# Kernel tuning notes

Measured on AMD Instinct MI355X. Metric: run time of the kernel, lower is better.

Reference implementation:

```python
import jax, jax.numpy as jnp
import numpy as np

N_NODES = 100000
N_EDGES = 3200000
D_IN = 512
D_OUT = 512


def setup_inputs() -> dict:
    key = jax.random.key(0)
    k1, k2, k3, k4, k5 = jax.random.split(key, 5)
    features = jax.random.normal(k1, (N_NODES, D_IN), dtype=jnp.float32)
    edge_src = jax.random.randint(k2, (N_EDGES,), 0, N_NODES, dtype=jnp.int32)
    edge_dst = jnp.sort(jax.random.randint(k3, (N_EDGES,), 0, N_NODES, dtype=jnp.int32))
    # normalized-adjacency-like positive edge weights
    edge_weight = jax.random.uniform(k4, (N_EDGES,), dtype=jnp.float32)
    # xavier_uniform_ for weight [D_IN, D_OUT]
    limit = float(np.sqrt(6.0 / (D_IN + D_OUT)))
    weight = jax.random.uniform(k5, (D_IN, D_OUT), dtype=jnp.float32,
                                minval=-limit, maxval=limit)
    return {
        "features": features,
        "weight": weight,
        "edge_src": edge_src,
        "edge_dst": edge_dst,
        "edge_weight": edge_weight,
        "times": 3,
    }


def reference(features, weight, edge_src, edge_dst, edge_weight, times):
    n_nodes = features.shape[0]
    # dense feature transform: support = features @ W
    support = features @ weight  # [N, D_OUT]

    def spmm(x):
        # out[dst] += w * x[src]  (one hop of sparse adjacency propagation)
        msgs = x[edge_src] * edge_weight[:, None]  # [E, D_OUT]
        return jax.ops.segment_sum(msgs, edge_dst, num_segments=n_nodes)

    output = spmm(support)
    for _ in range(times - 1):
        output = spmm(output)
    return output
```

## Files before the change

### kernel.cpp

```cpp
#include <hip/hip_runtime.h>

#define N_NODES_C 100000
#define N_EDGES_C 3200000
#define DDIM 512

typedef float v4f __attribute__((ext_vector_type(4)));
typedef unsigned int v4u __attribute__((ext_vector_type(4)));
typedef _Float16 v8hf __attribute__((ext_vector_type(8)));

__device__ inline unsigned short f2h(float f) {
    union { _Float16 h; unsigned short u; } v;
    v.h = (_Float16)f;
    return v.u;
}
__device__ inline float h2f(unsigned short s) {
    union { unsigned short u; _Float16 h; } v;
    v.u = s;
    return (float)v.h;
}

__device__ __forceinline__ void gload_lds16(const void* g, void* l) {
    __builtin_amdgcn_global_load_lds(
        (const __attribute__((address_space(1))) unsigned int*)(void*)(g),
        (__attribute__((address_space(3))) unsigned int*)(l),
        16, 0, 0);
}

__global__ __launch_bounds__(256) void build_rowptr(const int* __restrict__ dst,
                                                    int* __restrict__ rp) {
    int n = blockIdx.x * blockDim.x + threadIdx.x;
    if (n > N_NODES_C) return;
    int lo = 0, hi = N_EDGES_C;
    while (lo < hi) {
        int mid = (lo + hi) >> 1;
        if (dst[mid] < n) lo = mid + 1;
        else hi = mid;
    }
    rp[n] = lo;
}

__global__ __launch_bounds__(256) void convert_x(const v4f* __restrict__ X,
                                                 v4u* __restrict__ Xh) {
    const size_t i = (size_t)blockIdx.x * 256 + threadIdx.x;
    const v4f a = X[2 * i];
    const v4f b = X[2 * i + 1];
    v4u o;
    o.x = (unsigned)f2h(a.x) | ((unsigned)f2h(a.y) << 16);
    o.y = (unsigned)f2h(a.z) | ((unsigned)f2h(a.w) << 16);
    o.z = (unsigned)f2h(b.x) | ((unsigned)f2h(b.y) << 16);
    o.w = (unsigned)f2h(b.z) | ((unsigned)f2h(b.w) << 16);
    Xh[i] = o;
}

__global__ __launch_bounds__(256) void transpose_b(const float* __restrict__ B,
                                                   unsigned short* __restrict__ Bt) {
    __shared__ float t[32][33];
    const int bk = blockIdx.x * 32;
    const int bn = blockIdx.y * 32;
    const int x  = threadIdx.x & 31;
    const int y0 = threadIdx.x >> 5;
#pragma unroll
    for (int r = y0; r < 32; r += 8)
        t[r][x] = B[(size_t)(bk + r) * DDIM + bn + x];
    __syncthreads();
#pragma unroll
    for (int r = y0; r < 32; r += 8)
        Bt[(size_t)(bn + r) * DDIM + bk + x] = f2h(t[x][r]);
}

__global__ __launch_bounds__(256) void gemm3(const unsigned short* __restrict__ Ah,
                                             const unsigned short* __restrict__ Bt,
                                             unsigned short* __restrict__ C,
                                             int M) {
    __shared__ unsigned short sA[128 * 32];
    __shared__ unsigned short sB[128 * 32];

    const int tid  = threadIdx.x;
    const int lane = tid & 63;
    const int wave = tid >> 6;
    const int quad = lane >> 4;
    const int l16  = lane & 15;
    const int wr   = (wave >> 1) * 64;
    const int wc   = (wave & 1) * 64;
    const int m0   = blockIdx.x * 128;
    const int n0   = blockIdx.y * 128;

    int ar0 = m0 + (tid >> 2);
    int ar1 = ar0 + 64;
    if (ar0 >= M) ar0 = 0;
    if (ar1 >= M) ar1 = 0;
    const unsigned short* ga0 = Ah + (size_t)ar0 * DDIM + (tid & 3) * 8;
    const unsigned short* ga1 = Ah + (size_t)ar1 * DDIM + (tid & 3) * 8;
    const unsigned short* gb0 = Bt + (size_t)(n0 + (tid >> 2)) * DDIM + (tid & 3) * 8;
    const unsigned short* gb1 = gb0 + (size_t)64 * DDIM;
    unsigned short* la0 = &sA[wave * 512];
    unsigned short* la1 = &sA[2048 + wave * 512];
    unsigned short* lb0 = &sB[wave * 512];
    unsigned short* lb1 = &sB[2048 + wave * 512];

    v4f acc[4][4] = {};

    for (int k0 = 0; k0 < DDIM; k0 += 32) {
        gload_lds16(ga0 + k0, la0);
        gload_lds16(ga1 + k0, la1);
        gload_lds16(gb0 + k0, lb0);
        gload_lds16(gb1 + k0, lb1);
        __syncthreads();

        v8hf af[4], bf[4];
#pragma unroll
        for (int i = 0; i < 4; ++i)
            af[i] = *(const v8hf*)&sA[(wr + i * 16 + l16) * 32 + quad * 8];
#pragma unroll
        for (int j = 0; j < 4; ++j)
            bf[j] = *(const v8hf*)&sB[(wc + j * 16 + l16) * 32 + quad * 8];
#pragma unroll
        for (int i = 0; i < 4; ++i)
#pragma unroll
            for (int j = 0; j < 4; ++j)
                acc[i][j] = __builtin_amdgcn_mfma_f32_16x16x32_f16(
                    af[i], bf[j], acc[i][j], 0, 0, 0);
        __syncthreads();
    }

#pragma unroll
    for (int i = 0; i < 4; ++i) {
#pragma unroll
        for (int j = 0; j < 4; ++j) {
#pragma unroll
            for (int r = 0; r < 4; ++r) {
                const int rg = m0 + wr + i * 16 + quad * 4 + r;
                const int cg = n0 + wc + j * 16 + l16;
                if (rg < M) C[(size_t)rg * DDIM + cg] = f2h(acc[i][j][r]);
            }
        }
    }
}

__device__ inline void fma8(float* acc, float w, v4u v) {
#pragma unroll
    for (int q = 0; q < 4; ++q) {
        const unsigned int u = v[q];
        acc[2 * q]     = fmaf(w, h2f((unsigned short)(u & 0xffffu)), acc[2 * q]);
        acc[2 * q + 1] = fmaf(w, h2f((unsigned short)(u >> 16)),     acc[2 * q + 1]);
    }
}

template <bool OUT_F32>
__global__ __launch_bounds__(256) void spmm_f16(const v4u* __restrict__ x,
                                                const int* __restrict__ esrc,
                                                const float* __restrict__ ew,
                                                const int* __restrict__ rp,
                                                void* __restrict__ y) {
    const int wave = threadIdx.x >> 6;
    const int lane = threadIdx.x & 63;
    const int n = blockIdx.x * 4 + wave;
    const int s = rp[n];
    const int e = rp[n + 1];

    float a0[8] = {}, a1[8] = {}, a2[8] = {}, a3[8] = {};

    int i = s;
    for (; i + 3 < e; i += 4) {
        const int s0 = esrc[i];
        const int s1 = esrc[i + 1];
        const int s2 = esrc[i + 2];
        const int s3 = esrc[i + 3];
        const float w0 = ew[i];
        const float w1 = ew[i + 1];
        const float w2 = ew[i + 2];
        const float w3 = ew[i + 3];
        v4u v0 = x[(size_t)s0 * 64 + lane];
        v4u v1 = x[(size_t)s1 * 64 + lane];
        v4u v2 = x[(size_t)s2 * 64 + lane];
        v4u v3 = x[(size_t)s3 * 64 + lane];
        fma8(a0, w0, v0);
        fma8(a1, w1, v1);
        fma8(a2, w2, v2);
        fma8(a3, w3, v3);
    }
    for (; i < e; ++i) {
        const int sI = esrc[i];
        const float wI = ew[i];
        v4u vI = x[(size_t)sI * 64 + lane];
        fma8(a0, wI, vI);
    }

    float r[8];
#pragma unroll
    for (int q = 0; q < 8; ++q) r[q] = (a0[q] + a1[q]) + (a2[q] + a3[q]);

    if (OUT_F32) {
        float* yo = (float*)y;
        v4f o0 = {r[0], r[1], r[2], r[3]};
        v4f o1 = {r[4], r[5], r[6], r[7]};
        *(v4f*)&yo[(size_t)n * DDIM + lane * 8] = o0;
        *(v4f*)&yo[(size_t)n * DDIM + lane * 8 + 4] = o1;
    } else {
        v4u o;
        o.x = (unsigned int)f2h(r[0]) | ((unsigned int)f2h(r[1]) << 16);
        o.y = (unsigned int)f2h(r[2]) | ((unsigned int)f2h(r[3]) << 16);
        o.z = (unsigned int)f2h(r[4]) | ((unsigned int)f2h(r[5]) << 16);
        o.w = (unsigned int)f2h(r[6]) | ((unsigned int)f2h(r[7]) << 16);
        ((v4u*)y)[(size_t)n * 64 + lane] = o;
    }
}

extern "C" void kernel_launch(void* const* d_in, const int* in_sizes, int n_in,
                              void* d_out, int out_size, void* d_ws, size_t ws_size,
                              hipStream_t stream) {
    const float* features = (const float*)d_in[0];
    const float* weight   = (const float*)d_in[1];
    const int*   esrc     = (const int*)d_in[2];
    const int*   edst     = (const int*)d_in[3];
    const float* ew       = (const float*)d_in[4];

    float* out = (float*)d_out;
    char*  ws  = (char*)d_ws;

    int* rp = (int*)ws;
    size_t rp_bytes = ((size_t)(N_NODES_C + 1) * sizeof(int) + 511) & ~(size_t)511;
    unsigned short* S  = (unsigned short*)(ws + rp_bytes);
    unsigned short* Y  = S + (size_t)N_NODES_C * DDIM;
    unsigned short* Xh = Y;
    unsigned short* Bt = (unsigned short*)d_out;

    build_rowptr<<<(N_NODES_C + 256) / 256, 256, 0, stream>>>(edst, rp);

    convert_x<<<(N_NODES_C * DDIM / 8) / 256, 256, 0, stream>>>(
        (const v4f*)features, (v4u*)Xh);

    transpose_b<<<dim3(16, 16), 256, 0, stream>>>(weight, Bt);

    dim3 ggrid((N_NODES_C + 127) / 128, DDIM / 128);
    gemm3<<<ggrid, 256, 0, stream>>>(Xh, Bt, S, N_NODES_C);

    const int sgrid = N_NODES_C / 4;
    spmm_f16<false><<<sgrid, 256, 0, stream>>>((const v4u*)S, esrc, ew, rp, Y);
    spmm_f16<false><<<sgrid, 256, 0, stream>>>((const v4u*)Y, esrc, ew, rp, S);
    spmm_f16<true ><<<sgrid, 256, 0, stream>>>((const v4u*)S, esrc, ew, rp, out);
}
```

Measured before the change: 1.767 ms.

## Split SpMM feature dimension into two column halves for cache locality

Measured after the change: 1.898 ms. +7.4%, slower.

```diff
diff --git a/kernel.cpp b/kernel.cpp
--- a/kernel.cpp
+++ b/kernel.cpp
@@ -6,6 +6,7 @@
 
 typedef float v4f __attribute__((ext_vector_type(4)));
 typedef unsigned int v4u __attribute__((ext_vector_type(4)));
+typedef unsigned int v2u __attribute__((ext_vector_type(2)));
 typedef _Float16 v8hf __attribute__((ext_vector_type(8)));
 
 __device__ inline unsigned short f2h(float f) {
@@ -137,9 +138,9 @@
     }
 }
 
-__device__ inline void fma8(float* acc, float w, v4u v) {
-#pragma unroll
-    for (int q = 0; q < 4; ++q) {
+__device__ inline void fma4(float* acc, float w, v2u v) {
+#pragma unroll
+    for (int q = 0; q < 2; ++q) {
         const unsigned int u = v[q];
         acc[2 * q]     = fmaf(w, h2f((unsigned short)(u & 0xffffu)), acc[2 * q]);
         acc[2 * q + 1] = fmaf(w, h2f((unsigned short)(u >> 16)),     acc[2 * q + 1]);
@@ -147,62 +148,61 @@
 }
 
 template <bool OUT_F32>
-__global__ __launch_bounds__(256) void spmm_f16(const v4u* __restrict__ x,
-                                                const int* __restrict__ esrc,
-                                                const float* __restrict__ ew,
-                                                const int* __restrict__ rp,
-                                                void* __restrict__ y) {
+__global__ __launch_bounds__(256) void spmm_half(const v2u* __restrict__ x,
+                                                 const int* __restrict__ esrc,
+                                                 const float* __restrict__ ew,
+                                                 const int* __restrict__ rp,
+                                                 void* __restrict__ y,
+                                                 int half) {
     const int wave = threadIdx.x >> 6;
     const int lane = threadIdx.x & 63;
     const int n = blockIdx.x * 4 + wave;
     const int s = rp[n];
     const int e = rp[n + 1];
-
-    float a0[8] = {}, a1[8] = {}, a2[8] = {}, a3[8] = {};
+    const size_t hoff = (size_t)half * 64 + lane;
+
+    float a0[4] = {}, a1[4] = {}, a2[4] = {}, a3[4] = {};
 
     int i = s;
     for (; i + 3 < e; i += 4) {
-        const int s0 = esrc[i];
-        const int s1 = esrc[i + 1];
-        const int s2 = esrc[i + 2];
-        const int s3 = esrc[i + 3];
-        const float w0 = ew[i];
-        const float w1 = ew[i + 1];
-        const float w2 = ew[i + 2];
-        const float w3 = ew[i + 3];
-        v4u v0 = x[(size_t)s0 * 64 + lane];
-        v4u v1 = x[(size_t)s1 * 64 + lane];
-        v4u v2 = x[(size_t)s2 * 64 + lane];
-        v4u v3 = x[(size_t)s3 * 64 + lane];
-        fma8(a0, w0, v0);
-        fma8(a1, w1, v1);
-        fma8(a2, w2, v2);
-        fma8(a3, w3, v3);
+        const int s0 = __builtin_nontemporal_load(&esrc[i]);
+        const int s1 = __builtin_nontemporal_load(&esrc[i + 1]);
+        const int s2 = __builtin_nontemporal_load(&esrc[i + 2]);
+        const int s3 = __builtin_nontemporal_load(&esrc[i + 3]);
+        const float w0 = __builtin_nontemporal_load(&ew[i]);
+        const float w1 = __builtin_nontemporal_load(&ew[i + 1]);
+        const float w2 = __builtin_nontemporal_load(&ew[i + 2]);
+        const float w3 = __builtin_nontemporal_load(&ew[i + 3]);
+        v2u v0 = x[(size_t)s0 * 128 + hoff];
+        v2u v1 = x[(size_t)s1 * 128 + hoff];
+        v2u v2 = x[(size_t)s2 * 128 + hoff];
+        v2u v3 = x[(size_t)s3 * 128 + hoff];
+        fma4(a0, w0, v0);
+        fma4(a1, w1, v1);
+        fma4(a2, w2, v2);
+        fma4(a3, w3, v3);
     }
     for (; i < e; ++i) {
         const int sI = esrc[i];
         const float wI = ew[i];
-        v4u vI = x[(size_t)sI * 64 + lane];
-        fma8(a0, wI, vI);
-    }
-
-    float r[8];
-#pragma unroll
-    for (int q = 0; q < 8; ++q) r[q] = (a0[q] + a1[q]) + (a2[q] + a3[q]);
+        v2u vI = x[(size_t)sI * 128 + hoff];
+        fma4(a0, wI, vI);
+    }
+
+    float r[4];
+#pragma unroll
+    for (int q = 0; q < 4; ++q) r[q] = (a0[q] + a1[q]) + (a2[q] + a3[q]);
 
     if (OUT_F32) {
         float* yo = (float*)y;
-        v4f o0 = {r[0], r[1], r[2], r[3]};
-        v4f o1 = {r[4], r[5], r[6], r[7]};
-        *(v4f*)&yo[(size_t)n * DDIM + lane * 8] = o0;
-        *(v4f*)&yo[(size_t)n * DDIM + lane * 8 + 4] = o1;
+        v4f o = {r[0], r[1], r[2], r[3]};
+        __builtin_nontemporal_store(
+            o, (v4f*)&yo[(size_t)n * DDIM + (size_t)half * 256 + lane * 4]);
     } else {
-        v4u o;
+        v2u o;
         o.x = (unsigned int)f2h(r[0]) | ((unsigned int)f2h(r[1]) << 16);
         o.y = (unsigned int)f2h(r[2]) | ((unsigned int)f2h(r[3]) << 16);
-        o.z = (unsigned int)f2h(r[4]) | ((unsigned int)f2h(r[5]) << 16);
-        o.w = (unsigned int)f2h(r[6]) | ((unsigned int)f2h(r[7]) << 16);
-        ((v4u*)y)[(size_t)n * 64 + lane] = o;
+        ((v2u*)y)[(size_t)n * 128 + hoff] = o;
     }
 }
 
@@ -236,7 +236,10 @@
     gemm3<<<ggrid, 256, 0, stream>>>(Xh, Bt, S, N_NODES_C);
 
     const int sgrid = N_NODES_C / 4;
-    spmm_f16<false><<<sgrid, 256, 0, stream>>>((const v4u*)S, esrc, ew, rp, Y);
-    spmm_f16<false><<<sgrid, 256, 0, stream>>>((const v4u*)Y, esrc, ew, rp, S);
-    spmm_f16<true ><<<sgrid, 256, 0, stream>>>((const v4u*)S, esrc, ew, rp, out);
-}
+    for (int h = 0; h < 2; ++h)
+        spmm_half<false><<<sgrid, 256, 0, stream>>>((const v2u*)S, esrc, ew, rp, Y, h);
+    for (int h = 0; h < 2; ++h)
+        spmm_half<false><<<sgrid, 256, 0, stream>>>((const v2u*)Y, esrc, ew, rp, S, h);
+    for (int h = 0; h < 2; ++h)
+        spmm_half<true ><<<sgrid, 256, 0, stream>>>((const v2u*)S, esrc, ew, rp, out, h);
+}
```

## Widen GEMM tile to 128x256 with 8 waves; use nontemporal loads and stores in SpMM

Applied to the files above, without the earlier changes.

Result: slower. 1.835 ms (+3.9%).

```diff
diff --git a/kernel.cpp b/kernel.cpp
--- a/kernel.cpp
+++ b/kernel.cpp
@@ -68,41 +68,36 @@
         Bt[(size_t)(bn + r) * DDIM + bk + x] = f2h(t[x][r]);
 }
 
-__global__ __launch_bounds__(256) void gemm3(const unsigned short* __restrict__ Ah,
+__global__ __launch_bounds__(512) void gemm4(const unsigned short* __restrict__ Ah,
                                              const unsigned short* __restrict__ Bt,
                                              unsigned short* __restrict__ C,
                                              int M) {
     __shared__ unsigned short sA[128 * 32];
-    __shared__ unsigned short sB[128 * 32];
+    __shared__ unsigned short sB[256 * 32];
 
     const int tid  = threadIdx.x;
     const int lane = tid & 63;
     const int wave = tid >> 6;
     const int quad = lane >> 4;
     const int l16  = lane & 15;
-    const int wr   = (wave >> 1) * 64;
-    const int wc   = (wave & 1) * 64;
+    const int wr   = (wave >> 2) * 64;
+    const int wc   = (wave & 3) * 64;
     const int m0   = blockIdx.x * 128;
-    const int n0   = blockIdx.y * 128;
-
-    int ar0 = m0 + (tid >> 2);
-    int ar1 = ar0 + 64;
-    if (ar0 >= M) ar0 = 0;
-    if (ar1 >= M) ar1 = 0;
-    const unsigned short* ga0 = Ah + (size_t)ar0 * DDIM + (tid & 3) * 8;
-    const unsigned short* ga1 = Ah + (size_t)ar1 * DDIM + (tid & 3) * 8;
+    const int n0   = blockIdx.y * 256;
+
+    int ar = m0 + (tid >> 2);
+    if (ar >= M) ar = 0;
+    const unsigned short* ga  = Ah + (size_t)ar * DDIM + (tid & 3) * 8;
     const unsigned short* gb0 = Bt + (size_t)(n0 + (tid >> 2)) * DDIM + (tid & 3) * 8;
-    const unsigned short* gb1 = gb0 + (size_t)64 * DDIM;
-    unsigned short* la0 = &sA[wave * 512];
-    unsigned short* la1 = &sA[2048 + wave * 512];
+    const unsigned short* gb1 = gb0 + (size_t)128 * DDIM;
+    unsigned short* la  = &sA[wave * 512];
     unsigned short* lb0 = &sB[wave * 512];
-    unsigned short* lb1 = &sB[2048 + wave * 512];
+    unsigned short* lb1 = &sB[4096 + wave * 512];
 
     v4f acc[4][4] = {};
 
     for (int k0 = 0; k0 < DDIM; k0 += 32) {
-        gload_lds16(ga0 + k0, la0);
-        gload_lds16(ga1 + k0, la1);
+        gload_lds16(ga  + k0, la);
         gload_lds16(gb0 + k0, lb0);
         gload_lds16(gb1 + k0, lb1);
         __syncthreads();
@@ -162,14 +157,14 @@
 
     int i = s;
     for (; i + 3 < e; i += 4) {
-        const int s0 = esrc[i];
-        const int s1 = esrc[i + 1];
-        const int s2 = esrc[i + 2];
-        const int s3 = esrc[i + 3];
-        const float w0 = ew[i];
-        const float w1 = ew[i + 1];
-        const float w2 = ew[i + 2];
-        const float w3 = ew[i + 3];
+        const int s0 = __builtin_nontemporal_load(&esrc[i]);
+        const int s1 = __builtin_nontemporal_load(&esrc[i + 1]);
+        const int s2 = __builtin_nontemporal_load(&esrc[i + 2]);
+        const int s3 = __builtin_nontemporal_load(&esrc[i + 3]);
+        const float w0 = __builtin_nontemporal_load(&ew[i]);
+        const float w1 = __builtin_nontemporal_load(&ew[i + 1]);
+        const float w2 = __builtin_nontemporal_load(&ew[i + 2]);
+        const float w3 = __builtin_nontemporal_load(&ew[i + 3]);
         v4u v0 = x[(size_t)s0 * 64 + lane];
         v4u v1 = x[(size_t)s1 * 64 + lane];
         v4u v2 = x[(size_t)s2 * 64 + lane];
@@ -194,15 +189,15 @@
         float* yo = (float*)y;
         v4f o0 = {r[0], r[1], r[2], r[3]};
         v4f o1 = {r[4], r[5], r[6], r[7]};
-        *(v4f*)&yo[(size_t)n * DDIM + lane * 8] = o0;
-        *(v4f*)&yo[(size_t)n * DDIM + lane * 8 + 4] = o1;
+        __builtin_nontemporal_store(o0, (v4f*)&yo[(size_t)n * DDIM + lane * 8]);
+        __builtin_nontemporal_store(o1, (v4f*)&yo[(size_t)n * DDIM + lane * 8 + 4]);
     } else {
         v4u o;
         o.x = (unsigned int)f2h(r[0]) | ((unsigned int)f2h(r[1]) << 16);
         o.y = (unsigned int)f2h(r[2]) | ((unsigned int)f2h(r[3]) << 16);
         o.z = (unsigned int)f2h(r[4]) | ((unsigned int)f2h(r[5]) << 16);
         o.w = (unsigned int)f2h(r[6]) | ((unsigned int)f2h(r[7]) << 16);
-        ((v4u*)y)[(size_t)n * 64 + lane] = o;
+        __builtin_nontemporal_store(o, &((v4u*)y)[(size_t)n * 64 + lane]);
     }
 }
 
@@ -232,8 +227,8 @@
 
     transpose_b<<<dim3(16, 16), 256, 0, stream>>>(weight, Bt);
 
-    dim3 ggrid((N_NODES_C + 127) / 128, DDIM / 128);
-    gemm3<<<ggrid, 256, 0, stream>>>(Xh, Bt, S, N_NODES_C);
+    dim3 ggrid((N_NODES_C + 127) / 128, DDIM / 256);
+    gemm4<<<ggrid, 512, 0, stream>>>(Xh, Bt, S, N_NODES_C);
 
     const int sgrid = N_NODES_C / 4;
     spmm_f16<false><<<sgrid, 256, 0, stream>>>((const v4u*)S, esrc, ew, rp, Y);
```

## Double-buffer LDS in GEMM and widen tile to 128x256 with 512 threads

Applied to the files above, without the earlier changes.

New measurement: 1.757 ms. About the same (-0.5%).

```diff
diff --git a/kernel.cpp b/kernel.cpp
--- a/kernel.cpp
+++ b/kernel.cpp
@@ -68,52 +68,51 @@
         Bt[(size_t)(bn + r) * DDIM + bk + x] = f2h(t[x][r]);
 }
 
-__global__ __launch_bounds__(256) void gemm3(const unsigned short* __restrict__ Ah,
+__global__ __launch_bounds__(512) void gemm5(const unsigned short* __restrict__ Ah,
                                              const unsigned short* __restrict__ Bt,
                                              unsigned short* __restrict__ C,
                                              int M) {
-    __shared__ unsigned short sA[128 * 32];
-    __shared__ unsigned short sB[128 * 32];
+    __shared__ unsigned short sA[2][128 * 32];
+    __shared__ unsigned short sB[2][256 * 32];
 
     const int tid  = threadIdx.x;
     const int lane = tid & 63;
     const int wave = tid >> 6;
     const int quad = lane >> 4;
     const int l16  = lane & 15;
-    const int wr   = (wave >> 1) * 64;
-    const int wc   = (wave & 1) * 64;
+    const int wr   = (wave >> 2) * 64;
+    const int wc   = (wave & 3) * 64;
     const int m0   = blockIdx.x * 128;
-    const int n0   = blockIdx.y * 128;
-
-    int ar0 = m0 + (tid >> 2);
-    int ar1 = ar0 + 64;
-    if (ar0 >= M) ar0 = 0;
-    if (ar1 >= M) ar1 = 0;
-    const unsigned short* ga0 = Ah + (size_t)ar0 * DDIM + (tid & 3) * 8;
-    const unsigned short* ga1 = Ah + (size_t)ar1 * DDIM + (tid & 3) * 8;
+    const int n0   = blockIdx.y * 256;
+
+    int ar = m0 + (tid >> 2);
+    if (ar >= M) ar = 0;
+    const unsigned short* ga  = Ah + (size_t)ar * DDIM + (tid & 3) * 8;
     const unsigned short* gb0 = Bt + (size_t)(n0 + (tid >> 2)) * DDIM + (tid & 3) * 8;
-    const unsigned short* gb1 = gb0 + (size_t)64 * DDIM;
-    unsigned short* la0 = &sA[wave * 512];
-    unsigned short* la1 = &sA[2048 + wave * 512];
-    unsigned short* lb0 = &sB[wave * 512];
-    unsigned short* lb1 = &sB[2048 + wave * 512];
+    const unsigned short* gb1 = gb0 + (size_t)128 * DDIM;
 
     v4f acc[4][4] = {};
 
-    for (int k0 = 0; k0 < DDIM; k0 += 32) {
-        gload_lds16(ga0 + k0, la0);
-        gload_lds16(ga1 + k0, la1);
-        gload_lds16(gb0 + k0, lb0);
-        gload_lds16(gb1 + k0, lb1);
-        __syncthreads();
-
+    gload_lds16(ga,  &sA[0][wave * 512]);
+    gload_lds16(gb0, &sB[0][wave * 512]);
+    gload_lds16(gb1, &sB[0][4096 + wave * 512]);
+    __syncthreads();
+
+    int cur = 0;
+    for (int t = 0; t < 16; ++t) {
+        if (t < 15) {
+            const int k1 = (t + 1) * 32;
+            gload_lds16(ga  + k1, &sA[cur ^ 1][wave * 512]);
+            gload_lds16(gb0 + k1, &sB[cur ^ 1][wave * 512]);
+            gload_lds16(gb1 + k1, &sB[cur ^ 1][4096 + wave * 512]);
+        }
         v8hf af[4], bf[4];
 #pragma unroll
         for (int i = 0; i < 4; ++i)
-            af[i] = *(const v8hf*)&sA[(wr + i * 16 + l16) * 32 + quad * 8];
+            af[i] = *(const v8hf*)&sA[cur][(wr + i * 16 + l16) * 32 + quad * 8];
 #pragma unroll
         for (int j = 0; j < 4; ++j)
-            bf[j] = *(const v8hf*)&sB[(wc + j * 16 + l16) * 32 + quad * 8];
+            bf[j] = *(const v8hf*)&sB[cur][(wc + j * 16 + l16) * 32 + quad * 8];
 #pragma unroll
         for (int i = 0; i < 4; ++i)
 #pragma unroll
@@ -121,6 +120,7 @@
                 acc[i][j] = __builtin_amdgcn_mfma_f32_16x16x32_f16(
                     af[i], bf[j], acc[i][j], 0, 0, 0);
         __syncthreads();
+        cur ^= 1;
     }
 
 #pragma unroll
@@ -232,8 +232,8 @@
 
     transpose_b<<<dim3(16, 16), 256, 0, stream>>>(weight, Bt);
 
-    dim3 ggrid((N_NODES_C + 127) / 128, DDIM / 128);
-    gemm3<<<ggrid, 256, 0, stream>>>(Xh, Bt, S, N_NODES_C);
+    dim3 ggrid((N_NODES_C + 127) / 128, DDIM / 256);
+    gemm5<<<ggrid, 512, 0, stream>>>(Xh, Bt, S, N_NODES_C);
 
     const int sgrid = N_NODES_C / 4;
     spmm_f16<false><<<sgrid, 256, 0, stream>>>((const v4u*)S, esrc, ew, rp, Y);
```
